# Performance work log

Hardware: AMD Instinct MI355X
Metric: run time of the kernel (lower is better)

The kernel has to match this reference:

```python
import jax, jax.numpy as jnp
import numpy as np

BS = 32  # leaf block size
NUM_HOPS = 1  # ATTENTION_HOPS


def setup_inputs() -> dict:
    key = jax.random.key(0)
    ks = jax.random.split(key, 10)
    B, N, C, H = 1, 131072, 256, 4
    E = 8 * N
    x = jax.random.normal(ks[0], (B, N, C), dtype=jnp.float32)
    rows = jax.random.randint(ks[1], (E,), 0, N)
    offs = jax.random.randint(ks[2], (E,), 0, BS)
    cols = (rows // BS) * BS + offs  # in-block neighbors
    edge_index = jnp.stack([rows, cols]).astype(jnp.int64)
    edge_values = jax.random.normal(ks[3], (E,), dtype=jnp.float32)
    positions = jax.random.uniform(ks[4], (N, 3), dtype=jnp.float32)
    qkv_w = jax.random.normal(ks[5], (3 * C, C), dtype=jnp.float32) * 0.02
    qkv_b = jnp.zeros((3 * C,), dtype=jnp.float32)
    proj_w = jax.random.normal(ks[6], (C, C), dtype=jnp.float32) * 0.02
    proj_b = jnp.zeros((C,), dtype=jnp.float32)
    gate_w = jax.random.normal(ks[7], (H, 4), dtype=jnp.float32) * 0.01  # init std=0.01
    gate_b = jnp.zeros((H,), dtype=jnp.float32)
    return {"x": x, "edge_index": edge_index, "edge_values": edge_values,
            "positions": positions, "qkv_w": qkv_w, "qkv_b": qkv_b,
            "proj_w": proj_w, "proj_b": proj_b, "gate_w": gate_w, "gate_b": gate_b}


def _connectivity(edge_index, edge_values, positions, nb):
    rows, cols = edge_index[0], edge_index[1]
    br, bc = rows // BS, cols // BS
    in_block = (br == bc) & (br < nb)
    r_l, c_l = rows % BS, cols % BS
    b_safe = jnp.where(in_block, br, nb)  # out-of-range -> dropped by scatter
    dx = positions[cols] - positions[rows]            # [E,3]
    ef_flat = jnp.concatenate([dx, edge_values[:, None]], axis=1)  # [E,4]
    adj = jnp.zeros((nb, BS, BS), jnp.float32).at[b_safe, r_l, c_l].set(1.0, mode='drop')
    eye = jnp.eye(BS, dtype=jnp.float32)
    reachable = jnp.broadcast_to(eye[None], (nb, BS, BS))
    cur = adj
    for _ in range(NUM_HOPS):
        reachable = jnp.clip(reachable + cur, 0.0, 1.0)
        cur = jnp.matmul(cur, adj)
    attn_mask = jnp.concatenate([reachable, jnp.ones((nb, BS, 1), jnp.float32)], axis=2)
    edge_feats = jnp.zeros((nb, BS, BS + 1, 4), jnp.float32)
    edge_feats = edge_feats.at[b_safe, r_l, c_l, :].set(ef_flat, mode='drop')
    return attn_mask, edge_feats


def reference(x, edge_index, edge_values, positions, qkv_w, qkv_b, proj_w, proj_b, gate_w, gate_b):
    B, N, C = x.shape
    H = gate_w.shape[0]
    hd = C // H
    scale = hd ** -0.5
    nb = N // BS  # N chosen divisible by BS (no pad)
    attn_mask, edge_feats = _connectivity(edge_index, edge_values, positions, nb)

    x_blk = x.reshape(B, nb, BS, C)
    block_node = x_blk.mean(axis=2, keepdims=True)
    kv = jnp.concatenate([x_blk, block_node], axis=2)  # [B,nb,BS+1,C]
    qkv_q = x_blk @ qkv_w.T + qkv_b
    qkv_kv = kv @ qkv_w.T + qkv_b
    q = qkv_q[..., :C].reshape(B, nb, BS, H, hd)
    k = qkv_kv[..., C:2 * C].reshape(B, nb, BS + 1, H, hd)
    v = qkv_kv[..., 2 * C:].reshape(B, nb, BS + 1, H, hd)

    scores = jnp.einsum('bnqhd,bnkhd->bnqkh', q, k) * scale

    ar = jnp.arange(BS)
    bias_physics = edge_feats.at[:, :, BS, :].set(0.0).at[:, :, BS, 3].set(1.0)
    bias_physics = bias_physics.at[:, ar, ar, :].set(0.0).at[:, ar, ar, 3].set(1.0)

    scores = scores + bias_physics[None, ..., 3:4]
    mask = attn_mask[None, :, :, :, None]  # [1,nb,BS,BS+1,1]
    scores = jnp.where(mask == 0, -jnp.inf, scores)
    attn_probs = jax.nn.softmax(scores, axis=3)

    gate = bias_physics @ gate_w.T + gate_b  # [nb,BS,BS+1,H]
    gate = jnp.where(mask == 0, 0.0, gate[None])
    combined = attn_probs + gate

    x_out = jnp.einsum('bnqkh,bnkhd->bnqhd', combined, v).reshape(B, nb, BS, C)
    out = x_out.reshape(B, N, C) @ proj_w.T + proj_b
    return out
```

## Files before the change

### kernel.cpp

```cpp
#include <hip/hip_runtime.h>
#include <math.h>

#define BSZ 32
#define CH  256

typedef short  bf16x8 __attribute__((ext_vector_type(8)));
typedef float  f32x4  __attribute__((ext_vector_type(4)));
typedef unsigned short ushort_t;
typedef unsigned int   uint_t;

#define MFMA(a, b, c) __builtin_amdgcn_mfma_f32_16x16x32_bf16((a), (b), (c), 0, 0, 0)

__device__ __forceinline__ ushort_t f2b(float f) {
    uint_t u = __builtin_bit_cast(uint_t, f);
    uint_t r = (u + 0x7FFFu + ((u >> 16) & 1u)) >> 16;
    return (ushort_t)r;
}
__device__ __forceinline__ float b2f(ushort_t u) {
    uint_t v = ((uint_t)u) << 16;
    return __builtin_bit_cast(float, v);
}
__device__ __forceinline__ uint_t pk2(float a, float b) {
    return (uint_t)f2b(a) | ((uint_t)f2b(b) << 16);
}

__global__ void edge_win_kernel(const int* __restrict__ ei, int E, int nb,
                                int* __restrict__ win) {
    int e = blockIdx.x * blockDim.x + threadIdx.x;
    if (e >= E) return;
    int r = ei[e];
    int c = ei[E + e];
    int br = r >> 5, bc = c >> 5;
    if (br == bc && br < nb) {
        atomicMax(&win[br * (BSZ * BSZ) + (r & 31) * BSZ + (c & 31)], e);
    }
}

__global__ void pgate_kernel(const float* __restrict__ pos,
                             const float* __restrict__ gate_w,
                             float* __restrict__ pg, int N) {
    int n = blockIdx.x * 256 + threadIdx.x;
    int h = blockIdx.y;
    if (n >= N) return;
    pg[(size_t)h * N + n] = pos[n * 3 + 0] * gate_w[h * 4 + 0]
                          + pos[n * 3 + 1] * gate_w[h * 4 + 1]
                          + pos[n * 3 + 2] * gate_w[h * 4 + 2];
}

__global__ void wconv_kernel(const float* __restrict__ qkv_w,
                             const float* __restrict__ proj_w,
                             ushort_t* __restrict__ qkv_wf,
                             ushort_t* __restrict__ proj_wf) {
    int i = blockIdx.x * blockDim.x + threadIdx.x;
    int lane = i & 63, ks = (i >> 6) & 7, tile = i >> 9;
    int l15 = lane & 15, lg = lane >> 4;
    if (tile < 48) {
        const float* src = qkv_w + (size_t)(tile * 16 + l15) * 256 + ks * 32 + lg * 8;
        ushort_t* dst = qkv_wf + (size_t)i * 8;
        #pragma unroll
        for (int e = 0; e < 8; ++e) dst[e] = f2b(src[e]);
    }
    if (tile < 16) {
        const float* src = proj_w + (size_t)(tile * 16 + l15) * 256 + ks * 32 + lg * 8;
        ushort_t* dst = proj_wf + (size_t)i * 8;
        #pragma unroll
        for (int e = 0; e < 8; ++e) dst[e] = f2b(src[e]);
    }
}

#define LS_XB   0
#define LS_QS   32768
#define LS_KS   65536
#define LS_VS   98304
#define LS_TOT  131072

__global__ __launch_bounds__(512, 2)
void fused_attn(const float* __restrict__ x,
                const ushort_t* __restrict__ qkv_wf,
                const float* __restrict__ qkv_b,
                const int* __restrict__ win,
                const float* __restrict__ ev,
                const float* __restrict__ pg,
                const ushort_t* __restrict__ proj_wf,
                const float* __restrict__ proj_b,
                const float* __restrict__ gate_w,
                const float* __restrict__ gate_b,
                float* __restrict__ out, int N)
{
    __shared__ __align__(16) char smem[LS_TOT];
    ushort_t* xb   = (ushort_t*)(smem + LS_XB);
    ushort_t* comb = (ushort_t*)(smem + LS_XB);
    ushort_t* qs   = (ushort_t*)(smem + LS_QS);
    ushort_t* xo   = (ushort_t*)(smem + LS_QS);
    ushort_t* ksm  = (ushort_t*)(smem + LS_KS);
    ushort_t* vs   = (ushort_t*)(smem + LS_VS);

    const int t = threadIdx.x;
    const int w = t >> 6, lane = t & 63, l15 = lane & 15, lg = lane >> 4;
    const int bi = blockIdx.x;
    const int mbase = bi * 64;

    #pragma unroll
    for (int i = 0; i < 8; ++i) {
        int flat = i * 2048 + t * 4;
        int r = flat >> 8, c = flat & 255;
        float4 xv = *(const float4*)&x[(size_t)(mbase + r) * CH + c];
        uint2 wv; wv.x = pk2(xv.x, xv.y); wv.y = pk2(xv.z, xv.w);
        *(uint2*)&xb[r * 256 + (c ^ ((r & 7) << 3))] = wv;
    }
    __syncthreads();

    const int slB = (l15 & 7) << 3;
    const f32x4 zf = {0.f, 0.f, 0.f, 0.f};

    bf16x8 xf[8][4];
    #pragma unroll
    for (int ks = 0; ks < 8; ++ks) {
        int k0 = (ks * 32 + lg * 8) ^ slB;
        xf[ks][0] = *(const bf16x8*)&xb[l15 * 256 + k0];
        xf[ks][1] = *(const bf16x8*)&xb[(16 + l15) * 256 + k0];
        xf[ks][2] = *(const bf16x8*)&xb[(32 + l15) * 256 + k0];
        xf[ks][3] = *(const bf16x8*)&xb[(48 + l15) * 256 + k0];
    }

    bf16x8 wA[8], wB[8];

#define LOADT(dst, itv) { _Pragma("unroll")                                   \
        for (int ks_ = 0; ks_ < 8; ++ks_)                                     \
            dst[ks_] = *(const bf16x8*)(qkv_wf                                \
                + ((size_t)((((itv) * 8 + w) * 8) + ks_)) * 512 + lane * 8); }

#define TILE_COMPUTE(CUR, SW) { _Pragma("unroll")                             \
        for (int ks_ = 0; ks_ < 8; ++ks_) {                                   \
            if (SW) {                                                         \
                a0 = MFMA(CUR[ks_], xf[ks_][0], a0);                          \
                a1 = MFMA(CUR[ks_], xf[ks_][1], a1);                          \
                a2 = MFMA(CUR[ks_], xf[ks_][2], a2);                          \
                a3 = MFMA(CUR[ks_], xf[ks_][3], a3);                          \
            } else {                                                          \
                a0 = MFMA(xf[ks_][0], CUR[ks_], a0);                          \
                a1 = MFMA(xf[ks_][1], CUR[ks_], a1);                          \
                a2 = MFMA(xf[ks_][2], CUR[ks_], a2);                          \
                a3 = MFMA(xf[ks_][3], CUR[ks_], a3);                          \
            } } }

#define STORE_QK(ITV) {                                                       \
        int tt_ = (ITV) * 8 + w;                                              \
        f32x4 bv4_ = *(const f32x4*)&qkv_b[tt_ * 16 + lg * 4];                \
        ushort_t* dst_ = ((ITV) < 2) ? qs : ksm;                              \
        int tloc_ = ((ITV) < 2) ? tt_ : tt_ - 16;                             \
        f32x4 av_[4] = {a0, a1, a2, a3};                                      \
        _Pragma("unroll")                                                     \
        for (int m_ = 0; m_ < 4; ++m_) {                                      \
            f32x4 v_ = av_[m_] + bv4_;                                        \
            uint2 wv_; wv_.x = pk2(v_[0], v_[1]); wv_.y = pk2(v_[2], v_[3]);  \
            *(uint2*)&dst_[(m_ >> 1) * 8192 + (tloc_ * 2 + (m_ & 1)) * 256    \
                           + lane * 4] = wv_;                                 \
        } }

#define STORE_V(ITV) {                                                        \
        int tt_ = (ITV) * 8 + w;                                              \
        int vch_ = (tt_ - 32) * 16 + l15;                                     \
        float bv_ = qkv_b[512 + vch_];                                        \
        int swzv_ = (vch_ & 3) << 3;                                          \
        f32x4 av_[4] = {a0, a1, a2, a3};                                      \
        _Pragma("unroll")                                                     \
        for (int m_ = 0; m_ < 4; ++m_) {                                      \
            f32x4 v_ = av_[m_];                                               \
            uint2 wv_; wv_.x = pk2(v_[0] + bv_, v_[1] + bv_);                 \
            wv_.y = pk2(v_[2] + bv_, v_[3] + bv_);                            \
            int roff_ = (((m_ & 1) * 16 + lg * 4)) ^ swzv_;                   \
            *(uint2*)&vs[(m_ >> 1) * 8192 + vch_ * 32 + roff_] = wv_;         \
        } }

#define DO_TILE(ITV, CUR) {                                                   \
        f32x4 a0 = zf, a1 = zf, a2 = zf, a3 = zf;                             \
        if ((ITV) < 4) { TILE_COMPUTE(CUR, 1) STORE_QK(ITV) }                 \
        else           { TILE_COMPUTE(CUR, 0) STORE_V(ITV) } }

    LOADT(wA, 0); LOADT(wB, 1);
    DO_TILE(0, wA); LOADT(wA, 2);
    DO_TILE(1, wB); LOADT(wB, 3);
    DO_TILE(2, wA); LOADT(wA, 4);
    DO_TILE(3, wB); LOADT(wB, 5);
    DO_TILE(4, wA);
    DO_TILE(5, wB);

    const int gl = w >> 2, h = w & 3;
    const int cb = mbase + gl * 32;
    uint4  wv4[2][2];
    float4 pgc[2];
    float  pgr[2];
    #pragma unroll
    for (int qt = 0; qt < 2; ++qt) {
        int qi = qt * 16 + l15;
        wv4[qt][0] = *(const uint4*)&win[(size_t)(bi * 2 + gl) * 1024
                                         + qi * 32 + lg * 4];
        wv4[qt][1] = *(const uint4*)&win[(size_t)(bi * 2 + gl) * 1024
                                         + qi * 32 + 16 + lg * 4];
        pgr[qt] = pg[(size_t)h * N + cb + qi];
    }
    pgc[0] = *(const float4*)&pg[(size_t)h * N + cb + lg * 4];
    pgc[1] = *(const float4*)&pg[(size_t)h * N + cb + 16 + lg * 4];
    const float gw3v = gate_w[h * 4 + 3];
    const float gbv  = gate_b[h];
    const float g3b  = gw3v + gbv;

    __syncthreads();

    float evv[2][8];
    #pragma unroll
    for (int qt = 0; qt < 2; ++qt)
        #pragma unroll
        for (int kt = 0; kt < 2; ++kt) {
            const int* wp = (const int*)&wv4[qt][kt];
            #pragma unroll
            for (int j = 0; j < 4; ++j) {
                int e = wp[j];
                evv[qt][kt * 4 + j] = ev[e < 0 ? 0 : e];
            }
        }

    uint4 qld[2][2], kld[2][2];
    #pragma unroll
    for (int rt = 0; rt < 2; ++rt) {
        #pragma unroll
        for (int ks2 = 0; ks2 < 2; ++ks2) {
            int ttq = h * 4 + ks2 * 2 + (lg >> 1);
            int a0 = gl * 8192 + (ttq * 2 + rt) * 256 + ((lg & 1) * 32 + l15) * 4;
            uint2 u0 = *(const uint2*)&qs[a0];
            uint2 u1 = *(const uint2*)&qs[a0 + 64];
            qld[rt][ks2] = (uint4){u0.x, u0.y, u1.x, u1.y};
            uint2 w0 = *(const uint2*)&ksm[a0];
            uint2 w1 = *(const uint2*)&ksm[a0 + 64];
            kld[rt][ks2] = (uint4){w0.x, w0.y, w1.x, w1.y};
        }
    }
    bf16x8 vf[4];
    #pragma unroll
    for (int ct = 0; ct < 4; ++ct) {
        int off = (lg * 8) ^ ((l15 & 3) << 3);
        vf[ct] = *(const bf16x8*)&vs[gl * 8192
                                     + (h * 64 + ct * 16 + l15) * 32 + off];
    }
    __syncthreads();

    f32x4 s[2][2];
    #pragma unroll
    for (int qt = 0; qt < 2; ++qt) { s[qt][0] = zf; s[qt][1] = zf; }
    #pragma unroll
    for (int qt = 0; qt < 2; ++qt) {
        #pragma unroll
        for (int ks2 = 0; ks2 < 2; ++ks2) {
            bf16x8 qf = __builtin_bit_cast(bf16x8, qld[qt][ks2]);
            #pragma unroll
            for (int kt = 0; kt < 2; ++kt)
                s[qt][kt] = MFMA(__builtin_bit_cast(bf16x8, kld[kt][ks2]),
                                 qf, s[qt][kt]);
        }
    }

    #pragma unroll
    for (int qt = 0; qt < 2; ++qt) {
        int qi = qt * 16 + l15;
        float r[8], gt[8];
        float rawsum = 0.f;
        #pragma unroll
        for (int kt = 0; kt < 2; ++kt) {
            const int* wp = (const int*)&wv4[qt][kt];
            #pragma unroll
            for (int j = 0; j < 4; ++j) {
                int kj = kt * 16 + lg * 4 + j;
                bool fixed = (kj == qi);
                bool valid = wp[j] >= 0;
                float e3 = evv[qt][kt * 4 + j];
                float sb = fixed ? 1.0f : (valid ? e3 : -INFINITY);
                float pgcv = ((const float*)&pgc[kt])[j];
                float g = fixed ? g3b
                        : (valid ? (pgcv - pgr[qt] + e3 * gw3v + gbv) : 0.0f);
                float sraw = s[qt][kt][j];
                rawsum += sraw;
                r[kt * 4 + j]  = sraw * 0.125f + sb;
                gt[kt * 4 + j] = g;
            }
        }
        rawsum += __shfl_xor(rawsum, 16);
        rawsum += __shfl_xor(rawsum, 32);
        float r2 = rawsum * (0.125f / 32.0f) + 1.0f;

        float m = fmaxf(fmaxf(fmaxf(r[0], r[1]), fmaxf(r[2], r[3])),
                        fmaxf(fmaxf(r[4], r[5]), fmaxf(r[6], r[7])));
        m = fmaxf(m, r2);
        m = fmaxf(m, __shfl_xor(m, 16));
        m = fmaxf(m, __shfl_xor(m, 32));
        float sum = 0.f;
        #pragma unroll
        for (int i = 0; i < 8; ++i) { r[i] = __expf(r[i] - m); sum += r[i]; }
        sum += __shfl_xor(sum, 16);
        sum += __shfl_xor(sum, 32);
        float e2 = __expf(r2 - m);
        float inv = 1.0f / (sum + e2);
        float comb32 = e2 * inv + g3b;
        float cadd = comb32 * 0.03125f;
        int swz = (l15 & 3) << 3;
        #pragma unroll
        for (int kt = 0; kt < 2; ++kt) {
            int kj0 = kt * 16 + lg * 4;
            uint2 wv;
            wv.x = pk2(r[kt*4+0] * inv + gt[kt*4+0] + cadd,
                       r[kt*4+1] * inv + gt[kt*4+1] + cadd);
            wv.y = pk2(r[kt*4+2] * inv + gt[kt*4+2] + cadd,
                       r[kt*4+3] * inv + gt[kt*4+3] + cadd);
            *(uint2*)&comb[(gl * 4 + h) * 1024 + qi * 32 + (kj0 ^ swz)] = wv;
        }
    }

    bf16x8 cfr[2];
    #pragma unroll
    for (int qt = 0; qt < 2; ++qt) {
        int qi = qt * 16 + l15;
        int off = (lg * 8) ^ ((l15 & 3) << 3);
        cfr[qt] = *(const bf16x8*)&comb[(gl * 4 + h) * 1024 + qi * 32 + off];
    }
    #pragma unroll
    for (int ct = 0; ct < 4; ++ct) {
        #pragma unroll
        for (int qt = 0; qt < 2; ++qt) {
            f32x4 acc2 = zf;
            acc2 = MFMA(vf[ct], cfr[qt], acc2);
            int qi = qt * 16 + l15;
            uint2 wv;
            wv.x = pk2(acc2[0], acc2[1]);
            wv.y = pk2(acc2[2], acc2[3]);
            int c0 = h * 64 + ct * 16 + lg * 4;
            *(uint2*)&xo[gl * 8192 + qi * 256 + (c0 ^ ((l15 & 7) << 3))] = wv;
        }
    }
    __syncthreads();

    {
        const int slR = (l15 & 7) << 3;
        bf16x8 pw[2][8];
        #pragma unroll
        for (int i = 0; i < 2; ++i) {
            int pt = w * 2 + i;
            #pragma unroll
            for (int ks = 0; ks < 8; ++ks)
                pw[i][ks] = *(const bf16x8*)(proj_wf
                               + ((size_t)(pt * 8 + ks)) * 512 + lane * 8);
        }
        f32x4 pacc[2][4];
        #pragma unroll
        for (int i = 0; i < 2; ++i)
            #pragma unroll
            for (int rt = 0; rt < 4; ++rt) pacc[i][rt] = zf;
        #pragma unroll
        for (int ks = 0; ks < 8; ++ks) {
            int k0 = ks * 32 + lg * 8;
            #pragma unroll
            for (int rt = 0; rt < 4; ++rt) {
                bf16x8 bfr = *(const bf16x8*)&xo[(rt >> 1) * 8192
                                 + ((rt & 1) * 16 + l15) * 256 + (k0 ^ slR)];
                pacc[0][rt] = MFMA(pw[0][ks], bfr, pacc[0][rt]);
                pacc[1][rt] = MFMA(pw[1][ks], bfr, pacc[1][rt]);
            }
        }
        #pragma unroll
        for (int i = 0; i < 2; ++i) {
            int pt = w * 2 + i, n0 = pt * 16;
            f32x4 bv = *(const f32x4*)&proj_b[n0 + lg * 4];
            #pragma unroll
            for (int rt = 0; rt < 4; ++rt) {
                f32x4 o = pacc[i][rt] + bv;
                int row = mbase + (rt >> 1) * 32 + (rt & 1) * 16 + l15;
                *(f32x4*)&out[(size_t)row * 256 + n0 + lg * 4] = o;
            }
        }
    }
}

extern "C" void kernel_launch(void* const* d_in, const int* in_sizes, int n_in,
                              void* d_out, int out_size, void* d_ws, size_t ws_size,
                              hipStream_t stream) {
    const float* x      = (const float*)d_in[0];
    const int*   ei     = (const int*)  d_in[1];
    const float* ev     = (const float*)d_in[2];
    const float* pos    = (const float*)d_in[3];
    const float* qkv_w  = (const float*)d_in[4];
    const float* qkv_b  = (const float*)d_in[5];
    const float* proj_w = (const float*)d_in[6];
    const float* proj_b = (const float*)d_in[7];
    const float* gate_w = (const float*)d_in[8];
    const float* gate_b = (const float*)d_in[9];
    float* out = (float*)d_out;

    const int E  = in_sizes[2];
    const int N  = in_sizes[0] / CH;
    const int nb = N / BSZ;

    char* ws = (char*)d_ws;
    int*   win = (int*)ws;
    float* pg  = (float*)(ws + (size_t)nb * 4096);
    size_t off = (size_t)nb * 4096 + (size_t)4 * N * 4;
    ushort_t* qkv_wf  = (ushort_t*)(ws + off); off += 48 * 8 * 64 * 8 * 2;
    ushort_t* proj_wf = (ushort_t*)(ws + off); off += 16 * 8 * 64 * 8 * 2;

    hipMemsetAsync(win, 0xFF, (size_t)nb * 4096, stream);
    edge_win_kernel<<<(E + 255) / 256, 256, 0, stream>>>(ei, E, nb, win);
    pgate_kernel<<<dim3((N + 255) / 256, 4), 256, 0, stream>>>(pos, gate_w, pg, N);
    wconv_kernel<<<96, 256, 0, stream>>>(qkv_w, proj_w, qkv_wf, proj_wf);
    fused_attn<<<nb / 2, 512, 0, stream>>>(x, qkv_wf, qkv_b, win, ev, pg,
                                           proj_wf, proj_b, gate_w, gate_b,
                                           out, N);
}
```

Before: 241.3 us.

## Double fused attention block to 1024 threads, splitting per-wave work in half

The fused attention kernel now launches 1024 threads (16 waves) per block instead of 512. Each wave handles one query tile in the attention stage, one tile each of Q, K and V in the QKV projection, and one output tile in the final projection. Loads of window indices, gate terms and edge values are moved to the start, before the first barrier, so their latency overlaps the x staging. The intent is more waves in flight per block to hide latency and shorter per-wave serial chains. The 128 KB LDS per block still limits a CU to one block, and __launch_bounds__(1024,4) may force tighter register limits or spills.

```diff
diff --git a/kernel.cpp b/kernel.cpp
--- a/kernel.cpp
+++ b/kernel.cpp
@@ -74,7 +74,7 @@
 #define LS_VS   98304
 #define LS_TOT  131072
 
-__global__ __launch_bounds__(512, 2)
+__global__ __launch_bounds__(1024, 4)
 void fused_attn(const float* __restrict__ x,
                 const ushort_t* __restrict__ qkv_wf,
                 const float* __restrict__ qkv_b,
@@ -99,14 +99,39 @@
     const int w = t >> 6, lane = t & 63, l15 = lane & 15, lg = lane >> 4;
     const int bi = blockIdx.x;
     const int mbase = bi * 64;
-
-    #pragma unroll
-    for (int i = 0; i < 8; ++i) {
-        int flat = i * 2048 + t * 4;
+    const int gl = w >> 3, h = (w >> 1) & 3, qt = w & 1;
+    const int qi = qt * 16 + l15;
+    const int cb = mbase + gl * 32;
+
+    uint4 wv4[2];
+    wv4[0] = *(const uint4*)&win[(size_t)(bi * 2 + gl) * 1024 + qi * 32 + lg * 4];
+    wv4[1] = *(const uint4*)&win[(size_t)(bi * 2 + gl) * 1024 + qi * 32 + 16 + lg * 4];
+    float pgr = pg[(size_t)h * N + cb + qi];
+    float4 pgc[2];
+    pgc[0] = *(const float4*)&pg[(size_t)h * N + cb + lg * 4];
+    pgc[1] = *(const float4*)&pg[(size_t)h * N + cb + 16 + lg * 4];
+    const float gw3v = gate_w[h * 4 + 3];
+    const float gbv  = gate_b[h];
+    const float g3b  = gw3v + gbv;
+
+    #pragma unroll
+    for (int i = 0; i < 4; ++i) {
+        int flat = i * 4096 + t * 4;
         int r = flat >> 8, c = flat & 255;
         float4 xv = *(const float4*)&x[(size_t)(mbase + r) * CH + c];
         uint2 wv; wv.x = pk2(xv.x, xv.y); wv.y = pk2(xv.z, xv.w);
         *(uint2*)&xb[r * 256 + (c ^ ((r & 7) << 3))] = wv;
+    }
+
+    float evv[8];
+    #pragma unroll
+    for (int kt = 0; kt < 2; ++kt) {
+        const int* wp = (const int*)&wv4[kt];
+        #pragma unroll
+        for (int j = 0; j < 4; ++j) {
+            int e = wp[j];
+            evv[kt * 4 + j] = ev[e < 0 ? 0 : e];
+        }
     }
     __syncthreads();
 
@@ -123,117 +148,89 @@
         xf[ks][3] = *(const bf16x8*)&xb[(48 + l15) * 256 + k0];
     }
 
-    bf16x8 wA[8], wB[8];
-
-#define LOADT(dst, itv) { _Pragma("unroll")                                   \
+    bf16x8 wA[8], wB[8], wC[8];
+
+#define LOADT(dst, tile) { _Pragma("unroll")                                  \
         for (int ks_ = 0; ks_ < 8; ++ks_)                                     \
             dst[ks_] = *(const bf16x8*)(qkv_wf                                \
-                + ((size_t)((((itv) * 8 + w) * 8) + ks_)) * 512 + lane * 8); }
-
-#define TILE_COMPUTE(CUR, SW) { _Pragma("unroll")                             \
-        for (int ks_ = 0; ks_ < 8; ++ks_) {                                   \
-            if (SW) {                                                         \
-                a0 = MFMA(CUR[ks_], xf[ks_][0], a0);                          \
-                a1 = MFMA(CUR[ks_], xf[ks_][1], a1);                          \
-                a2 = MFMA(CUR[ks_], xf[ks_][2], a2);                          \
-                a3 = MFMA(CUR[ks_], xf[ks_][3], a3);                          \
-            } else {                                                          \
-                a0 = MFMA(xf[ks_][0], CUR[ks_], a0);                          \
-                a1 = MFMA(xf[ks_][1], CUR[ks_], a1);                          \
-                a2 = MFMA(xf[ks_][2], CUR[ks_], a2);                          \
-                a3 = MFMA(xf[ks_][3], CUR[ks_], a3);                          \
-            } } }
-
-#define STORE_QK(ITV) {                                                       \
-        int tt_ = (ITV) * 8 + w;                                              \
-        f32x4 bv4_ = *(const f32x4*)&qkv_b[tt_ * 16 + lg * 4];                \
-        ushort_t* dst_ = ((ITV) < 2) ? qs : ksm;                              \
-        int tloc_ = ((ITV) < 2) ? tt_ : tt_ - 16;                             \
-        f32x4 av_[4] = {a0, a1, a2, a3};                                      \
-        _Pragma("unroll")                                                     \
-        for (int m_ = 0; m_ < 4; ++m_) {                                      \
-            f32x4 v_ = av_[m_] + bv4_;                                        \
-            uint2 wv_; wv_.x = pk2(v_[0], v_[1]); wv_.y = pk2(v_[2], v_[3]);  \
-            *(uint2*)&dst_[(m_ >> 1) * 8192 + (tloc_ * 2 + (m_ & 1)) * 256    \
-                           + lane * 4] = wv_;                                 \
-        } }
-
-#define STORE_V(ITV) {                                                        \
-        int tt_ = (ITV) * 8 + w;                                              \
-        int vch_ = (tt_ - 32) * 16 + l15;                                     \
-        float bv_ = qkv_b[512 + vch_];                                        \
-        int swzv_ = (vch_ & 3) << 3;                                          \
-        f32x4 av_[4] = {a0, a1, a2, a3};                                      \
-        _Pragma("unroll")                                                     \
-        for (int m_ = 0; m_ < 4; ++m_) {                                      \
-            f32x4 v_ = av_[m_];                                               \
-            uint2 wv_; wv_.x = pk2(v_[0] + bv_, v_[1] + bv_);                 \
-            wv_.y = pk2(v_[2] + bv_, v_[3] + bv_);                            \
-            int roff_ = (((m_ & 1) * 16 + lg * 4)) ^ swzv_;                   \
-            *(uint2*)&vs[(m_ >> 1) * 8192 + vch_ * 32 + roff_] = wv_;         \
-        } }
-
-#define DO_TILE(ITV, CUR) {                                                   \
-        f32x4 a0 = zf, a1 = zf, a2 = zf, a3 = zf;                             \
-        if ((ITV) < 4) { TILE_COMPUTE(CUR, 1) STORE_QK(ITV) }                 \
-        else           { TILE_COMPUTE(CUR, 0) STORE_V(ITV) } }
-
-    LOADT(wA, 0); LOADT(wB, 1);
-    DO_TILE(0, wA); LOADT(wA, 2);
-    DO_TILE(1, wB); LOADT(wB, 3);
-    DO_TILE(2, wA); LOADT(wA, 4);
-    DO_TILE(3, wB); LOADT(wB, 5);
-    DO_TILE(4, wA);
-    DO_TILE(5, wB);
-
-    const int gl = w >> 2, h = w & 3;
-    const int cb = mbase + gl * 32;
-    uint4  wv4[2][2];
-    float4 pgc[2];
-    float  pgr[2];
-    #pragma unroll
-    for (int qt = 0; qt < 2; ++qt) {
-        int qi = qt * 16 + l15;
-        wv4[qt][0] = *(const uint4*)&win[(size_t)(bi * 2 + gl) * 1024
-                                         + qi * 32 + lg * 4];
-        wv4[qt][1] = *(const uint4*)&win[(size_t)(bi * 2 + gl) * 1024
-                                         + qi * 32 + 16 + lg * 4];
-        pgr[qt] = pg[(size_t)h * N + cb + qi];
-    }
-    pgc[0] = *(const float4*)&pg[(size_t)h * N + cb + lg * 4];
-    pgc[1] = *(const float4*)&pg[(size_t)h * N + cb + 16 + lg * 4];
-    const float gw3v = gate_w[h * 4 + 3];
-    const float gbv  = gate_b[h];
-    const float g3b  = gw3v + gbv;
-
+                + ((size_t)((tile) * 8 + ks_)) * 512 + lane * 8); }
+
+    LOADT(wA, w);
+    LOADT(wB, 16 + w);
+
+    {
+        f32x4 a0 = zf, a1 = zf, a2 = zf, a3 = zf;
+        #pragma unroll
+        for (int ks = 0; ks < 8; ++ks) {
+            a0 = MFMA(wA[ks], xf[ks][0], a0);
+            a1 = MFMA(wA[ks], xf[ks][1], a1);
+            a2 = MFMA(wA[ks], xf[ks][2], a2);
+            a3 = MFMA(wA[ks], xf[ks][3], a3);
+        }
+        f32x4 bv4 = *(const f32x4*)&qkv_b[w * 16 + lg * 4];
+        f32x4 av[4] = {a0 + bv4, a1 + bv4, a2 + bv4, a3 + bv4};
+        #pragma unroll
+        for (int m = 0; m < 4; ++m) {
+            uint2 wv; wv.x = pk2(av[m][0], av[m][1]); wv.y = pk2(av[m][2], av[m][3]);
+            *(uint2*)&qs[(m >> 1) * 8192 + (w * 2 + (m & 1)) * 256 + lane * 4] = wv;
+        }
+    }
+    LOADT(wC, 32 + w);
+    {
+        f32x4 a0 = zf, a1 = zf, a2 = zf, a3 = zf;
+        #pragma unroll
+        for (int ks = 0; ks < 8; ++ks) {
+            a0 = MFMA(wB[ks], xf[ks][0], a0);
+            a1 = MFMA(wB[ks], xf[ks][1], a1);
+            a2 = MFMA(wB[ks], xf[ks][2], a2);
+            a3 = MFMA(wB[ks], xf[ks][3], a3);
+        }
+        f32x4 bv4 = *(const f32x4*)&qkv_b[256 + w * 16 + lg * 4];
+        f32x4 av[4] = {a0 + bv4, a1 + bv4, a2 + bv4, a3 + bv4};
+        #pragma unroll
+        for (int m = 0; m < 4; ++m) {
+            uint2 wv; wv.x = pk2(av[m][0], av[m][1]); wv.y = pk2(av[m][2], av[m][3]);
+            *(uint2*)&ksm[(m >> 1) * 8192 + (w * 2 + (m & 1)) * 256 + lane * 4] = wv;
+        }
+    }
+    {
+        f32x4 a0 = zf, a1 = zf, a2 = zf, a3 = zf;
+        #pragma unroll
+        for (int ks = 0; ks < 8; ++ks) {
+            a0 = MFMA(xf[ks][0], wC[ks], a0);
+            a1 = MFMA(xf[ks][1], wC[ks], a1);
+            a2 = MFMA(xf[ks][2], wC[ks], a2);
+            a3 = MFMA(xf[ks][3], wC[ks], a3);
+        }
+        int vch = w * 16 + l15;
+        float bv = qkv_b[512 + vch];
+        int swzv = (vch & 3) << 3;
+        f32x4 av[4] = {a0, a1, a2, a3};
+        #pragma unroll
+        for (int m = 0; m < 4; ++m) {
+            uint2 wv; wv.x = pk2(av[m][0] + bv, av[m][1] + bv);
+            wv.y = pk2(av[m][2] + bv, av[m][3] + bv);
+            int roff = (((m & 1) * 16 + lg * 4)) ^ swzv;
+            *(uint2*)&vs[(m >> 1) * 8192 + vch * 32 + roff] = wv;
+        }
+    }
     __syncthreads();
 
-    float evv[2][8];
-    #pragma unroll
-    for (int qt = 0; qt < 2; ++qt)
+    uint4 qld[2], kld[2][2];
+    #pragma unroll
+    for (int ks2 = 0; ks2 < 2; ++ks2) {
+        int ttq = h * 4 + ks2 * 2 + (lg >> 1);
+        int lo = ((lg & 1) * 32 + l15) * 4;
+        int aq = gl * 8192 + (ttq * 2 + qt) * 256 + lo;
+        uint2 u0 = *(const uint2*)&qs[aq];
+        uint2 u1 = *(const uint2*)&qs[aq + 64];
+        qld[ks2] = (uint4){u0.x, u0.y, u1.x, u1.y};
         #pragma unroll
         for (int kt = 0; kt < 2; ++kt) {
-            const int* wp = (const int*)&wv4[qt][kt];
-            #pragma unroll
-            for (int j = 0; j < 4; ++j) {
-                int e = wp[j];
-                evv[qt][kt * 4 + j] = ev[e < 0 ? 0 : e];
-            }
-        }
-
-    uint4 qld[2][2], kld[2][2];
-    #pragma unroll
-    for (int rt = 0; rt < 2; ++rt) {
-        #pragma unroll
-        for (int ks2 = 0; ks2 < 2; ++ks2) {
-            int ttq = h * 4 + ks2 * 2 + (lg >> 1);
-            int a0 = gl * 8192 + (ttq * 2 + rt) * 256 + ((lg & 1) * 32 + l15) * 4;
-            uint2 u0 = *(const uint2*)&qs[a0];
-            uint2 u1 = *(const uint2*)&qs[a0 + 64];
-            qld[rt][ks2] = (uint4){u0.x, u0.y, u1.x, u1.y};
-            uint2 w0 = *(const uint2*)&ksm[a0];
-            uint2 w1 = *(const uint2*)&ksm[a0 + 64];
-            kld[rt][ks2] = (uint4){w0.x, w0.y, w1.x, w1.y};
+            int ak = gl * 8192 + (ttq * 2 + kt) * 256 + lo;
+            uint2 w0 = *(const uint2*)&ksm[ak];
+            uint2 w1 = *(const uint2*)&ksm[ak + 64];
+            kld[kt][ks2] = (uint4){w0.x, w0.y, w1.x, w1.y};
         }
     }
     bf16x8 vf[4];
@@ -245,40 +242,33 @@
     }
     __syncthreads();
 
-    f32x4 s[2][2];
-    #pragma unroll
-    for (int qt = 0; qt < 2; ++qt) { s[qt][0] = zf; s[qt][1] = zf; }
-    #pragma unroll
-    for (int qt = 0; qt < 2; ++qt) {
-        #pragma unroll
-        for (int ks2 = 0; ks2 < 2; ++ks2) {
-            bf16x8 qf = __builtin_bit_cast(bf16x8, qld[qt][ks2]);
-            #pragma unroll
-            for (int kt = 0; kt < 2; ++kt)
-                s[qt][kt] = MFMA(__builtin_bit_cast(bf16x8, kld[kt][ks2]),
-                                 qf, s[qt][kt]);
-        }
-    }
-
-    #pragma unroll
-    for (int qt = 0; qt < 2; ++qt) {
-        int qi = qt * 16 + l15;
+    f32x4 s[2];
+    s[0] = zf; s[1] = zf;
+    #pragma unroll
+    for (int ks2 = 0; ks2 < 2; ++ks2) {
+        bf16x8 qf = __builtin_bit_cast(bf16x8, qld[ks2]);
+        #pragma unroll
+        for (int kt = 0; kt < 2; ++kt)
+            s[kt] = MFMA(__builtin_bit_cast(bf16x8, kld[kt][ks2]), qf, s[kt]);
+    }
+
+    {
         float r[8], gt[8];
         float rawsum = 0.f;
         #pragma unroll
         for (int kt = 0; kt < 2; ++kt) {
-            const int* wp = (const int*)&wv4[qt][kt];
+            const int* wp = (const int*)&wv4[kt];
             #pragma unroll
             for (int j = 0; j < 4; ++j) {
                 int kj = kt * 16 + lg * 4 + j;
                 bool fixed = (kj == qi);
                 bool valid = wp[j] >= 0;
-                float e3 = evv[qt][kt * 4 + j];
+                float e3 = evv[kt * 4 + j];
                 float sb = fixed ? 1.0f : (valid ? e3 : -INFINITY);
                 float pgcv = ((const float*)&pgc[kt])[j];
                 float g = fixed ? g3b
-                        : (valid ? (pgcv - pgr[qt] + e3 * gw3v + gbv) : 0.0f);
-                float sraw = s[qt][kt][j];
+                        : (valid ? (pgcv - pgr + e3 * gw3v + gbv) : 0.0f);
+                float sraw = s[kt][j];
                 rawsum += sraw;
                 r[kt * 4 + j]  = sraw * 0.125f + sb;
                 gt[kt * 4 + j] = g;
@@ -315,45 +305,33 @@
         }
     }
 
-    bf16x8 cfr[2];
-    #pragma unroll
-    for (int qt = 0; qt < 2; ++qt) {
-        int qi = qt * 16 + l15;
+    bf16x8 cfr;
+    {
         int off = (lg * 8) ^ ((l15 & 3) << 3);
-        cfr[qt] = *(const bf16x8*)&comb[(gl * 4 + h) * 1024 + qi * 32 + off];
+        cfr = *(const bf16x8*)&comb[(gl * 4 + h) * 1024 + qi * 32 + off];
     }
     #pragma unroll
     for (int ct = 0; ct < 4; ++ct) {
-        #pragma unroll
-        for (int qt = 0; qt < 2; ++qt) {
-            f32x4 acc2 = zf;
-            acc2 = MFMA(vf[ct], cfr[qt], acc2);
-            int qi = qt * 16 + l15;
-            uint2 wv;
-            wv.x = pk2(acc2[0], acc2[1]);
-            wv.y = pk2(acc2[2], acc2[3]);
-            int c0 = h * 64 + ct * 16 + lg * 4;
-            *(uint2*)&xo[gl * 8192 + qi * 256 + (c0 ^ ((l15 & 7) << 3))] = wv;
-        }
+        f32x4 acc2 = zf;
+        acc2 = MFMA(vf[ct], cfr, acc2);
+        uint2 wv;
+        wv.x = pk2(acc2[0], acc2[1]);
+        wv.y = pk2(acc2[2], acc2[3]);
+        int c0 = h * 64 + ct * 16 + lg * 4;
+        *(uint2*)&xo[gl * 8192 + qi * 256 + (c0 ^ ((l15 & 7) << 3))] = wv;
     }
     __syncthreads();
 
     {
         const int slR = (l15 & 7) << 3;
-        bf16x8 pw[2][8];
-        #pragma unroll
-        for (int i = 0; i < 2; ++i) {
-            int pt = w * 2 + i;
-            #pragma unroll
-            for (int ks = 0; ks < 8; ++ks)
-                pw[i][ks] = *(const bf16x8*)(proj_wf
-                               + ((size_t)(pt * 8 + ks)) * 512 + lane * 8);
-        }
-        f32x4 pacc[2][4];
-        #pragma unroll
-        for (int i = 0; i < 2; ++i)
-            #pragma unroll
-            for (int rt = 0; rt < 4; ++rt) pacc[i][rt] = zf;
+        bf16x8 pw[8];
+        #pragma unroll
+        for (int ks = 0; ks < 8; ++ks)
+            pw[ks] = *(const bf16x8*)(proj_wf
+                        + ((size_t)(w * 8 + ks)) * 512 + lane * 8);
+        f32x4 pacc[4];
+        #pragma unroll
+        for (int rt = 0; rt < 4; ++rt) pacc[rt] = zf;
         #pragma unroll
         for (int ks = 0; ks < 8; ++ks) {
             int k0 = ks * 32 + lg * 8;
@@ -361,20 +339,16 @@
             for (int rt = 0; rt < 4; ++rt) {
                 bf16x8 bfr = *(const bf16x8*)&xo[(rt >> 1) * 8192
                                  + ((rt & 1) * 16 + l15) * 256 + (k0 ^ slR)];
-                pacc[0][rt] = MFMA(pw[0][ks], bfr, pacc[0][rt]);
-                pacc[1][rt] = MFMA(pw[1][ks], bfr, pacc[1][rt]);
+                pacc[rt] = MFMA(pw[ks], bfr, pacc[rt]);
             }
         }
-        #pragma unroll
-        for (int i = 0; i < 2; ++i) {
-            int pt = w * 2 + i, n0 = pt * 16;
-            f32x4 bv = *(const f32x4*)&proj_b[n0 + lg * 4];
-            #pragma unroll
-            for (int rt = 0; rt < 4; ++rt) {
-                f32x4 o = pacc[i][rt] + bv;
-                int row = mbase + (rt >> 1) * 32 + (rt & 1) * 16 + l15;
-                *(f32x4*)&out[(size_t)row * 256 + n0 + lg * 4] = o;
-            }
+        int n0 = w * 16;
+        f32x4 bv = *(const f32x4*)&proj_b[n0 + lg * 4];
+        #pragma unroll
+        for (int rt = 0; rt < 4; ++rt) {
+            f32x4 o = pacc[rt] + bv;
+            int row = mbase + (rt >> 1) * 32 + (rt & 1) * 16 + l15;
+            *(f32x4*)&out[(size_t)row * 256 + n0 + lg * 4] = o;
         }
     }
 }
@@ -409,7 +383,7 @@
     edge_win_kernel<<<(E + 255) / 256, 256, 0, stream>>>(ei, E, nb, win);
     pgate_kernel<<<dim3((N + 255) / 256, 4), 256, 0, stream>>>(pos, gate_w, pg, N);
     wconv_kernel<<<96, 256, 0, stream>>>(qkv_w, proj_w, qkv_wf, proj_wf);
-    fused_attn<<<nb / 2, 512, 0, stream>>>(x, qkv_wf, qkv_b, win, ev, pg,
-                                           proj_wf, proj_b, gate_w, gate_b,
-                                           out, N);
-}
+    fused_attn<<<nb / 2, 1024, 0, stream>>>(x, qkv_wf, qkv_b, win, ev, pg,
+                                            proj_wf, proj_b, gate_w, gate_b,
+                                            out, N);
+}
```

Measured after the change: 247.4 us. 2.5% more time.
